# Kernel optimization log

Hardware: AMD Instinct MI355X
Metric: run time of the kernel (lower is better)

## Reference

```python
import jax, jax.numpy as jnp
import numpy as np

B, H, W_SP, C = 256, 14, 14, 768
NUM_CLASSES = 701


def setup_inputs() -> dict:
    key = jax.random.key(0)
    k1, k2, k3 = jax.random.split(key, 3)
    x1 = jax.random.normal(k1, (B, H, W_SP, C), dtype=jnp.float32)
    x2 = jax.random.normal(k2, (B, H, W_SP, C), dtype=jnp.float32)
    W = jax.random.normal(k3, (C, NUM_CLASSES), dtype=jnp.float32) * 0.02
    b = jnp.zeros((NUM_CLASSES,), dtype=jnp.float32)
    return {"x1": x1, "x2": x2, "W": W, "b": b}


def _sgm(feats):
    """Vectorized SGM: per-sample sort by normalized token energy, gap-based
    split index, masked means for background/foreground. feats: [B, N, C]."""
    n = feats.shape[1]
    M = feats.sum(axis=-1)                                  # [B, N] token energies
    mn = M.min(axis=-1, keepdims=True)
    mx = M.max(axis=-1, keepdims=True)
    Mn = (M - mn) / (mx - mn)                               # normalized to [0,1]
    order = jnp.argsort(Mn, axis=-1)                        # ascending
    sorted_tens = jnp.take_along_axis(feats, order[:, :, None], axis=1)  # [B,N,C]
    sorted_M = jnp.take_along_axis(Mn, order, axis=-1)      # [B, N]
    # diff[j] = M[j+1]-M[j], forced to 0 where M[j]==0 (as in original)
    diff = jnp.where(sorted_M[:, :-1] == 0.0, 0.0,
                     sorted_M[:, 1:] - sorted_M[:, :-1])    # [B, N-1]
    k = jnp.argmax(diff, axis=-1)                           # [B] split index
    idx = jnp.arange(n)[None, :]                            # [1, N]
    fg_mask = (idx < k[:, None]).astype(feats.dtype)        # rows [:k] -> foreground
    bg_mask = 1.0 - fg_mask                                 # rows [k:] -> background
    fg_cnt = jnp.maximum(k.astype(feats.dtype), 1.0)[:, None]
    bg_cnt = jnp.maximum((n - k).astype(feats.dtype), 1.0)[:, None]
    foregr = jnp.einsum('bnc,bn->bc', sorted_tens, fg_mask) / fg_cnt
    backgr = jnp.einsum('bnc,bn->bc', sorted_tens, bg_mask) / bg_cnt
    return backgr, foregr


def reference(x1, x2, W, b):
    # flatten spatial dims into a token axis: [B, H*W, C]
    f1 = x1.reshape(x1.shape[0], -1, x1.shape[-1])
    f2 = x2.reshape(x2.shape[0], -1, x2.shape[-1])
    x1_bg, x1_fg = _sgm(f1)
    x2_bg, x2_fg = _sgm(f2)
    classif = lambda v: v @ W + b
    return (classif(x1_bg), classif(x1_fg), classif(x2_bg), classif(x2_fg))
```

## Files before the change

### kernel.cpp

```cpp
#include <hip/hip_runtime.h>
#include <hip/hip_bf16.h>

#define NTOK 196
#define QTOK 49
#define CDIM 768
#define BSAMP 256
#define NTASK 512
#define NCLS 701
#define NCLSP 704

typedef __attribute__((ext_vector_type(8))) short bf16x8;
typedef __attribute__((ext_vector_type(4))) float f32x4;

__device__ __forceinline__ void add4(float4& a, const float4& b) {
  a.x += b.x; a.y += b.y; a.z += b.z; a.w += b.w;
}

__global__ __launch_bounds__(256, 8) void phaseA_kernel(const float* __restrict__ x1,
                                                        const float* __restrict__ x2,
                                                        float* __restrict__ Mg,
                                                        float* __restrict__ Sg) {
  const int b    = blockIdx.x;
  const int task = b >> 2;
  const int q    = b & 3;
  const int s    = task & 255;
  const int br   = task >> 8;
  const float* __restrict__ feats = (br ? x2 : x1) + (size_t)s * (NTOK * CDIM);

  const int tid  = threadIdx.x;
  const int lane = tid & 63;
  const int wv   = tid >> 6;

  __shared__ float colred[4][CDIM];

  float4 a0 = {0,0,0,0}, a1 = {0,0,0,0}, a2 = {0,0,0,0};
  const float* lanebase = feats + (size_t)(q * QTOK) * CDIM + lane * 4;

  for (int tl = wv; tl < QTOK; tl += 4) {
    const float* p = lanebase + (size_t)tl * CDIM;
    const float4 r0 = *(const float4*)(p);
    const float4 r1 = *(const float4*)(p + 256);
    const float4 r2 = *(const float4*)(p + 512);
    add4(a0, r0); add4(a1, r1); add4(a2, r2);
    float e = ((r0.x + r0.y) + (r0.z + r0.w))
            + ((r1.x + r1.y) + (r1.z + r1.w))
            + ((r2.x + r2.y) + (r2.z + r2.w));
    #pragma unroll
    for (int off = 32; off; off >>= 1) e += __shfl_xor(e, off);
    if (lane == 0) Mg[(size_t)task * NTOK + q * QTOK + tl] = e;
  }

  *(float4*)&colred[wv][lane * 4      ] = a0;
  *(float4*)&colred[wv][lane * 4 + 256] = a1;
  *(float4*)&colred[wv][lane * 4 + 512] = a2;
  __syncthreads();
  for (int c = tid; c < CDIM; c += 256) {
    Sg[(size_t)b * CDIM + c] = (colred[0][c] + colred[1][c])
                             + (colred[2][c] + colred[3][c]);
  }
}

__global__ __launch_bounds__(256) void sgm2_kernel(const float* __restrict__ x1,
                                                   const float* __restrict__ x2,
                                                   const float* __restrict__ Mg,
                                                   const float* __restrict__ Sg,
                                                   __hip_bfloat16* __restrict__ Vb) {
  const int task = blockIdx.x;
  const int s  = task & 255;
  const int br = task >> 8;
  const float* __restrict__ feats = (br ? x2 : x1) + (size_t)s * (NTOK * CDIM);

  const int tid  = threadIdx.x;
  const int lane = tid & 63;
  const int wv   = tid >> 6;

  __shared__ float Msh[NTOK];
  __shared__ float Mn[NTOK];
  __shared__ float sortedv[NTOK];
  __shared__ int   rnk[NTOK];
  __shared__ int   list[NTOK];
  __shared__ float redmin[4], redmax[4];
  __shared__ int   kSh;
  __shared__ int   cntSh;
  __shared__ float partT[4][CDIM];

  if (tid < NTOK) Msh[tid] = Mg[(size_t)task * NTOK + tid];
  if (tid == 0) cntSh = 0;

  float srow[3];
  #pragma unroll
  for (int j = 0; j < 3; j++) {
    const int c = tid + j * 256;
    const float* sq = Sg + (size_t)(task * 4) * CDIM + c;
    srow[j] = (sq[0] + sq[CDIM]) + (sq[2 * CDIM] + sq[3 * CDIM]);
  }
  __syncthreads();

  float vmn = (tid < NTOK) ? Msh[tid] :  1e30f;
  float vmx = (tid < NTOK) ? Msh[tid] : -1e30f;
  #pragma unroll
  for (int off = 32; off; off >>= 1) {
    vmn = fminf(vmn, __shfl_xor(vmn, off));
    vmx = fmaxf(vmx, __shfl_xor(vmx, off));
  }
  if (lane == 0) { redmin[wv] = vmn; redmax[wv] = vmx; }
  __syncthreads();
  float mn = redmin[0], mx = redmax[0];
  #pragma unroll
  for (int i = 1; i < 4; i++) { mn = fminf(mn, redmin[i]); mx = fmaxf(mx, redmax[i]); }
  const float rng = mx - mn;
  if (tid < NTOK) Mn[tid] = (Msh[tid] - mn) / rng;
  __syncthreads();

  if (tid < NTOK) {
    const float mv = Mn[tid];
    int r = 0;
    for (int u = 0; u < NTOK; u++) {
      const float o = Mn[u];
      r += (o < mv) || (o == mv && u < tid);
    }
    sortedv[r] = mv;
    rnk[tid] = r;
  }
  __syncthreads();

  if (tid < 64) {
    float bd = -1.0f; int bj = NTOK;
    for (int j = lane; j < NTOK - 1; j += 64) {
      const float sj = sortedv[j];
      const float d = (sj == 0.0f) ? 0.0f : (sortedv[j + 1] - sj);
      if (d > bd || (d == bd && j < bj)) { bd = d; bj = j; }
    }
    #pragma unroll
    for (int off = 32; off; off >>= 1) {
      const float od = __shfl_xor(bd, off);
      const int   oj = __shfl_xor(bj, off);
      if (od > bd || (od == bd && oj < bj)) { bd = od; bj = oj; }
    }
    if (lane == 0) kSh = bj;
  }
  __syncthreads();

  const int k = kSh;
  const bool takeFg = (k <= NTOK / 2);

  if (tid < NTOK) {
    const int r = rnk[tid];
    const bool inSet = takeFg ? (r < k) : (r >= k);
    if (inSet) { int p = atomicAdd(&cntSh, 1); list[p] = tid; }
  }
  __syncthreads();
  const int m = cntSh;

  float4 t0a = {0,0,0,0}, t1a = {0,0,0,0}, t2a = {0,0,0,0};
  const float* lanebase = feats + lane * 4;
  for (int i0 = wv * 4; i0 < m; i0 += 16) {
    const int nb = m - i0;
    float4 r[4][3];
    #pragma unroll
    for (int j = 0; j < 4; j++) {
      if (j < nb) {
        const int tk = list[i0 + j];
        const float* p = lanebase + (size_t)tk * CDIM;
        #pragma unroll
        for (int g = 0; g < 3; g++) r[j][g] = *(const float4*)(p + g * 256);
      }
    }
    #pragma unroll
    for (int j = 0; j < 4; j++) {
      if (j < nb) { add4(t0a, r[j][0]); add4(t1a, r[j][1]); add4(t2a, r[j][2]); }
    }
  }

  *(float4*)&partT[wv][lane * 4      ] = t0a;
  *(float4*)&partT[wv][lane * 4 + 256] = t1a;
  *(float4*)&partT[wv][lane * 4 + 512] = t2a;
  __syncthreads();

  const float fgc = (float)(k > 1 ? k : 1);
  const float bgc = (float)((NTOK - k) > 1 ? (NTOK - k) : 1);
  const size_t rowFg = (size_t)(2 * br + 1) * BSAMP + s;
  const size_t rowBg = (size_t)(2 * br    ) * BSAMP + s;
  #pragma unroll
  for (int j = 0; j < 3; j++) {
    const int c = tid + j * 256;
    const float T = (partT[0][c] + partT[1][c]) + (partT[2][c] + partT[3][c]);
    const float S = srow[j];
    float fg, bg;
    if (takeFg) { fg = T;     bg = S - T; }
    else        { bg = T;     fg = S - T; }
    Vb[rowFg * CDIM + c] = __float2bfloat16(fg / fgc);
    Vb[rowBg * CDIM + c] = __float2bfloat16(bg / bgc);
  }
}

__global__ __launch_bounds__(256) void wt_kernel(const float* __restrict__ W,
                                                 __hip_bfloat16* __restrict__ WT) {
  __shared__ float tile[32][33];
  const int c0 = blockIdx.x * 32;
  const int k0 = blockIdx.y * 32;
  const int tx = threadIdx.x & 31;
  const int ty = threadIdx.x >> 5;
  #pragma unroll
  for (int i = 0; i < 4; i++) {
    const int kr = ty + i * 8;
    const int c = c0 + tx;
    tile[kr][tx] = (c < NCLS) ? W[(size_t)(k0 + kr) * NCLS + c] : 0.0f;
  }
  __syncthreads();
  #pragma unroll
  for (int i = 0; i < 4; i++) {
    const int cr = ty + i * 8;
    const int cls = c0 + cr;
    WT[(size_t)cls * CDIM + k0 + tx] = __float2bfloat16(tile[tx][cr]);
  }
}

__global__ __launch_bounds__(256) void mfma_gemm(const __hip_bfloat16* __restrict__ Vb,
                                                 const __hip_bfloat16* __restrict__ WT,
                                                 const float* __restrict__ bias,
                                                 float* __restrict__ out) {
  const int w = blockIdx.x * 4 + (threadIdx.x >> 6);
  const int lane = threadIdx.x & 63;
  const int tr = w / (NCLSP / 16);
  const int tc = w % (NCLSP / 16);
  const int m0 = tr * 16;
  const int n0 = tc * 16;
  const int ko = (lane >> 4) * 8;

  const short* aptr = (const short*)Vb + (size_t)(m0 + (lane & 15)) * CDIM + ko;
  const short* bptr = (const short*)WT + (size_t)(n0 + (lane & 15)) * CDIM + ko;

  f32x4 acc = {0.f, 0.f, 0.f, 0.f};
  #pragma unroll
  for (int k0 = 0; k0 < CDIM; k0 += 32) {
    const bf16x8 af = *(const bf16x8*)(aptr + k0);
    const bf16x8 bf = *(const bf16x8*)(bptr + k0);
    acc = __builtin_amdgcn_mfma_f32_16x16x32_bf16(af, bf, acc, 0, 0, 0);
  }

  const int crow = m0 + (lane >> 4) * 4;
  const int ccol = n0 + (lane & 15);
  if (ccol < NCLS) {
    const float bv = bias[ccol];
    #pragma unroll
    for (int r = 0; r < 4; r++)
      out[(size_t)(crow + r) * NCLS + ccol] = acc[r] + bv;
  }
}

extern "C" void kernel_launch(void* const* d_in, const int* in_sizes, int n_in,
                              void* d_out, int out_size, void* d_ws, size_t ws_size,
                              hipStream_t stream) {
  const float* x1 = (const float*)d_in[0];
  const float* x2 = (const float*)d_in[1];
  const float* W  = (const float*)d_in[2];
  const float* b  = (const float*)d_in[3];
  float* out = (float*)d_out;

  char* ws = (char*)d_ws;
  __hip_bfloat16* Vb = (__hip_bfloat16*)ws;
  __hip_bfloat16* WT = (__hip_bfloat16*)(ws + 1572864);
  float* Mg = (float*)(ws + 1572864 + 1081344);
  float* Sg = (float*)(ws + 1572864 + 1081344 + 401408);

  phaseA_kernel<<<2048, 256, 0, stream>>>(x1, x2, Mg, Sg);
  sgm2_kernel<<<512, 256, 0, stream>>>(x1, x2, Mg, Sg, Vb);
  wt_kernel<<<dim3(22, 24), 256, 0, stream>>>(W, WT);
  mfma_gemm<<<704, 256, 0, stream>>>(Vb, WT, b, out);
}
```

Measured before the change: 353.3 us.

## Stream phaseA token rows through LDS with async global_load_lds pipeline

Replaces the direct float4 global loads in the token-energy/column-sum kernel with per-wave asynchronous global-to-LDS DMA into a 4-slot ring buffer, keeping three rows in flight and using explicit vmcnt waits. Energies are staged in shared memory and written out coalesced after the barrier. This aims to keep more memory requests outstanding per wave, but the larger LDS footprint forces the occupancy hint down from 8 to 2 blocks, which may reduce latency hiding from other waves.

```diff
diff --git a/kernel.cpp b/kernel.cpp
--- a/kernel.cpp
+++ b/kernel.cpp
@@ -5,18 +5,24 @@
 #define QTOK 49
 #define CDIM 768
 #define BSAMP 256
-#define NTASK 512
 #define NCLS 701
 #define NCLSP 704
 
 typedef __attribute__((ext_vector_type(8))) short bf16x8;
 typedef __attribute__((ext_vector_type(4))) float f32x4;
 
+typedef __attribute__((address_space(1))) const unsigned char gas_u8;
+typedef __attribute__((address_space(3))) unsigned char las_u8;
+
+__device__ __forceinline__ void dma16(const void* g, void* l) {
+  __builtin_amdgcn_global_load_lds((gas_u8*)g, (las_u8*)l, 16, 0, 0);
+}
+
 __device__ __forceinline__ void add4(float4& a, const float4& b) {
   a.x += b.x; a.y += b.y; a.z += b.z; a.w += b.w;
 }
 
-__global__ __launch_bounds__(256, 8) void phaseA_kernel(const float* __restrict__ x1,
+__global__ __launch_bounds__(256, 2) void phaseA_kernel(const float* __restrict__ x1,
                                                         const float* __restrict__ x2,
                                                         float* __restrict__ Mg,
                                                         float* __restrict__ Sg) {
@@ -26,34 +32,56 @@
   const int s    = task & 255;
   const int br   = task >> 8;
   const float* __restrict__ feats = (br ? x2 : x1) + (size_t)s * (NTOK * CDIM);
+  const char*  qbase = (const char*)(feats + (size_t)(q * QTOK) * CDIM);
 
   const int tid  = threadIdx.x;
   const int lane = tid & 63;
   const int wv   = tid >> 6;
 
+  __shared__ __align__(16) char stage[4 * 4 * 3072];
+  __shared__ float Men[QTOK + 3];
   __shared__ float colred[4][CDIM];
 
-  float4 a0 = {0,0,0,0}, a1 = {0,0,0,0}, a2 = {0,0,0,0};
-  const float* lanebase = feats + (size_t)(q * QTOK) * CDIM + lane * 4;
-
-  for (int tl = wv; tl < QTOK; tl += 4) {
-    const float* p = lanebase + (size_t)tl * CDIM;
-    const float4 r0 = *(const float4*)(p);
-    const float4 r1 = *(const float4*)(p + 256);
-    const float4 r2 = *(const float4*)(p + 512);
-    add4(a0, r0); add4(a1, r1); add4(a2, r2);
+  char* wstage = stage + wv * (4 * 3072);
+  const int n = (wv == 0) ? 13 : 12;
+
+  float4 acc0 = {0,0,0,0}, acc1 = {0,0,0,0}, acc2 = {0,0,0,0};
+
+  auto issue = [&](int j) {
+    const char* g = qbase + (size_t)(wv + 4 * j) * (CDIM * 4) + lane * 16;
+    char* l = wstage + (j & 3) * 3072;
+    dma16(g,        l);
+    dma16(g + 1024, l + 1024);
+    dma16(g + 2048, l + 2048);
+  };
+
+  issue(0); issue(1); issue(2);
+  for (int j = 0; j < n; ++j) {
+    if (j + 3 < n) issue(j + 3);
+    const int rem = n - 1 - j;
+    if (rem >= 3)      __builtin_amdgcn_s_waitcnt(0x0F79);
+    else if (rem == 2) __builtin_amdgcn_s_waitcnt(0x0F76);
+    else if (rem == 1) __builtin_amdgcn_s_waitcnt(0x0F73);
+    else               __builtin_amdgcn_s_waitcnt(0x0F70);
+
+    const char* lb = wstage + (j & 3) * 3072 + lane * 16;
+    const float4 r0 = *(const float4*)(lb);
+    const float4 r1 = *(const float4*)(lb + 1024);
+    const float4 r2 = *(const float4*)(lb + 2048);
+    add4(acc0, r0); add4(acc1, r1); add4(acc2, r2);
     float e = ((r0.x + r0.y) + (r0.z + r0.w))
             + ((r1.x + r1.y) + (r1.z + r1.w))
             + ((r2.x + r2.y) + (r2.z + r2.w));
     #pragma unroll
     for (int off = 32; off; off >>= 1) e += __shfl_xor(e, off);
-    if (lane == 0) Mg[(size_t)task * NTOK + q * QTOK + tl] = e;
-  }
-
-  *(float4*)&colred[wv][lane * 4      ] = a0;
-  *(float4*)&colred[wv][lane * 4 + 256] = a1;
-  *(float4*)&colred[wv][lane * 4 + 512] = a2;
-  __syncthreads();
+    if (lane == 0) Men[wv + 4 * j] = e;
+  }
+
+  *(float4*)&colred[wv][lane * 4      ] = acc0;
+  *(float4*)&colred[wv][lane * 4 + 256] = acc1;
+  *(float4*)&colred[wv][lane * 4 + 512] = acc2;
+  __syncthreads();
+  if (tid < QTOK) Mg[(size_t)task * NTOK + q * QTOK + tid] = Men[tid];
   for (int c = tid; c < CDIM; c += 256) {
     Sg[(size_t)b * CDIM + c] = (colred[0][c] + colred[1][c])
                              + (colred[2][c] + colred[3][c]);
```

Measured after the change: 355.1 us. No clear change (+0.5%).
